# Kernel optimization log

Measured on AMD Instinct MI355X. Metric: run time of the kernel, lower is better.

The kernel has to match this reference:

```python
import jax, jax.numpy as jnp
import numpy as np

B, N, F_IN, F_OUT = 8, 2048, 128, 64
ALPHA = 0.2  # LeakyReLU negative slope
NEG_BIG = -9e15


def setup_inputs() -> dict:
    key = jax.random.key(0)
    k_h, k_adj, k_W, k_a = jax.random.split(key, 4)
    h = jax.random.normal(k_h, (B, N, F_IN), dtype=jnp.float32)
    adj = jax.random.bernoulli(k_adj, 0.1, (N, N)).astype(jnp.float32)
    adj = jnp.maximum(adj, jnp.eye(N, dtype=jnp.float32))
    # xavier_uniform with gain=1.414
    def xavier(k, shape, gain=1.414):
        fan_in, fan_out = shape[0], shape[1]
        bound = gain * np.sqrt(6.0 / (fan_in + fan_out))
        return jax.random.uniform(k, shape, jnp.float32, -bound, bound)
    W = xavier(k_W, (F_IN, F_OUT))
    a = xavier(k_a, (2 * F_OUT, 1))
    return {"h": h, "adj": adj, "W": W, "a": a}


def reference(h, adj, W, a):
    # Wh: [B, N, F_out]
    Wh = jnp.matmul(h, W)
    # a = [a1; a2]; e_ij = leakyrelu(a1.Wh_i + a2.Wh_j) == original concat+matmul
    a1 = a[:F_OUT, 0]
    a2 = a[F_OUT:, 0]
    f = jnp.einsum('bnf,f->bn', Wh, a1)  # [B, N] source term
    g = jnp.einsum('bnf,f->bn', Wh, a2)  # [B, N] target term
    e = jax.nn.leaky_relu(f[:, :, None] + g[:, None, :], negative_slope=ALPHA)  # [B,N,N]
    scores = jnp.where(adj[None, :, :] > 0, e, jnp.float32(NEG_BIG))
    attention = jax.nn.softmax(scores, axis=2)
    # dropout is identity in eval mode (training=False)
    h_prime = jnp.matmul(attention, Wh)  # [B, N, F_out]
    return h_prime
```

## Files before the change

kernel.cpp:

```cpp
#include <hip/hip_runtime.h>
#include <hip/hip_bf16.h>
#include <math.h>

#define B 8
#define N 2048
#define F_IN 128
#define F_OUT 64
#define ALPHA 0.2f

typedef _Float16 half8 __attribute__((ext_vector_type(8)));
typedef float f32x4 __attribute__((ext_vector_type(4)));

__global__ __launch_bounds__(256) void bitmask_kernel(
    const float* __restrict__ adj, unsigned* __restrict__ bits,
    const float* __restrict__ W, const float* __restrict__ a,
    _Float16* __restrict__ Wfrag, float* __restrict__ wa)
{
    const int i = blockIdx.x;
    const int tid = threadIdx.x;
    const int lane = tid & 63;
    const int w = tid >> 6;
    const float* row = adj + (size_t)i * N;
#pragma unroll
    for (int jt = 0; jt < 8; ++jt) {
        float v = row[jt * 256 + tid];
        unsigned long long m = __ballot(v > 0.f);
        if (lane == 0) {
            bits[i * 64 + jt * 8 + w * 2]     = (unsigned)m;
            bits[i * 64 + jt * 8 + w * 2 + 1] = (unsigned)(m >> 32);
        }
    }

    if (blockIdx.x == 0) {
#pragma unroll
        for (int u = 0; u < 32; ++u) {
            int o    = tid * 32 + u;
            int slot = o & 7;
            int ln   = (o >> 3) & 63;
            int fg   = (o >> 9) & 3;
            int ks   = o >> 11;
            int k    = ks * 32 + (ln >> 4) * 8 + slot;
            int f    = fg * 16 + (ln & 15);
            Wfrag[o] = (_Float16)W[k * 64 + f];
        }
        const int k = tid & 127;
        const float* ap = a + (tid >> 7) * 64;
        float s = 0.f;
#pragma unroll
        for (int f = 0; f < 64; ++f) s += W[k * 64 + f] * ap[f];
        wa[(tid >> 7) * 128 + k] = s;
    }
}

__global__ __launch_bounds__(256) void wh_fg_t_kernel(
    const float* __restrict__ h, const _Float16* __restrict__ Wfrag,
    const float* __restrict__ wa, _Float16* __restrict__ Wpack,
    float* __restrict__ fv, float* __restrict__ gv)
{
    const int tid  = threadIdx.x;
    const int w    = tid >> 6;
    const int lane = tid & 63;
    const int mrow = lane & 15;
    const int quad = lane >> 4;

    __shared__ float hs[16 * 132];

    const float4* h4 = (const float4*)(h + (size_t)blockIdx.x * 16 * F_IN);
#pragma unroll
    for (int s = 0; s < 2; ++s) {
        int idx = s * 256 + tid;
        *(float4*)&hs[(idx >> 5) * 132 + (idx & 31) * 4] = h4[idx];
    }

    half8 wF[4];
#pragma unroll
    for (int ks = 0; ks < 4; ++ks)
        wF[ks] = *(const half8*)(Wfrag + (((ks * 4 + w) * 64) + lane) * 8);

    __syncthreads();

    const int jgl = blockIdx.x * 16;
    const int b   = jgl >> 11;
    const int jb  = jgl & (N - 1);
    const float* hrow = &hs[mrow * 132];

    f32x4 acc = {0.f, 0.f, 0.f, 0.f};
#pragma unroll
    for (int ks = 0; ks < 4; ++ks) {
        const float* hp = hrow + ks * 32 + quad * 8;
        float4 x0 = *(const float4*)hp;
        float4 x1 = *(const float4*)(hp + 4);
        half8 aF;
#pragma unroll
        for (int t = 0; t < 4; ++t) {
            aF[t]     = (_Float16)((const float*)&x0)[t];
            aF[4 + t] = (_Float16)((const float*)&x1)[t];
        }
        acc = __builtin_amdgcn_mfma_f32_16x16x32_f16(aF, wF[ks], acc, 0, 0, 0);
    }

    if (w == 0) {
        const float* hp = hrow + quad * 32;
        const float* w1 = wa + quad * 32;
        const float* w2 = wa + 128 + quad * 32;
        float s1 = 0.f, s2 = 0.f;
#pragma unroll
        for (int t = 0; t < 32; ++t) {
            float hv = hp[t];
            s1 += hv * w1[t];
            s2 += hv * w2[t];
        }
        s1 += __shfl_xor(s1, 16, 64); s1 += __shfl_xor(s1, 32, 64);
        s2 += __shfl_xor(s2, 16, 64); s2 += __shfl_xor(s2, 32, 64);
        if (lane < 16) {
            fv[(size_t)b * N + jb + lane] = s1;
            gv[(size_t)b * N + jb + lane] = s2;
        }
    }

    const int m     = jb >> 7;
    const int q     = (jb >> 5) & 3;
    const int jg    = (jb & 31) + quad * 4;
    const int flane = ((jg >> 3) & 3) * 16 + mrow;
    const int slot  = jg & 7;
    _Float16* base = Wpack + ((((size_t)b * 16 + m) * 4 + q) * 4 + w) * 512
                     + (size_t)flane * 8 + slot;
    union { _Float16 hh[4]; ushort4 u; } pk;
#pragma unroll
    for (int reg = 0; reg < 4; ++reg) pk.hh[reg] = (_Float16)acc[reg];
    *(ushort4*)(base) = pk.u;
}

#define MSTR 68
#define RSTR 68

__global__ __launch_bounds__(256) void attn_mfma_kernel(
    const _Float16* __restrict__ Wpack, const float* __restrict__ fv,
    const float* __restrict__ gv, const unsigned* __restrict__ bits,
    float* __restrict__ out)
{
    const int i0 = blockIdx.x * 32;
    const int b  = blockIdx.y;
    const int tid  = threadIdx.x;
    const int lane = tid & 63;
    const int wsl  = tid >> 6;
    const int mrow = lane & 15;
    const int quad = lane >> 4;

    __shared__ __align__(16) float    gs[N];
    __shared__ float    fs[32];
    __shared__ float    ms[32];
    __shared__ __align__(16) unsigned mws[32 * MSTR];
    __shared__ float    redacc[4 * 32 * RSTR];
    __shared__ float    rsp[4 * 32];

    const float4* g4 = (const float4*)(gv + (size_t)b * N);
    ((float4*)gs)[tid]       = g4[tid];
    ((float4*)gs)[tid + 256] = g4[tid + 256];
    if (tid < 32) fs[tid] = fv[(size_t)b * N + i0 + tid];
#pragma unroll
    for (int s = 0; s < 2; ++s) {
        const int idx = tid + s * 256;
        const int i   = idx >> 4;
        const int w4  = (idx & 15) * 4;
        *(uint4*)&mws[i * MSTR + w4] =
            *(const uint4*)&bits[(size_t)(i0 + i) * 64 + w4];
    }
    __syncthreads();

#pragma unroll
    for (int rr = 0; rr < 2; ++rr) {
        const int ii = rr * 16 + (tid >> 4);
        const int jj = tid & 15;
        float gmax = -INFINITY;
#pragma unroll
        for (int t = 0; t < 4; ++t) {
            unsigned mw = mws[ii * MSTR + jj * 4 + t];
            const int jb = jj * 128 + t * 32;
            while (mw) {
                int bit = __builtin_ctz(mw);
                gmax = fmaxf(gmax, gs[jb + bit]);
                mw &= mw - 1;
            }
        }
#pragma unroll
        for (int off = 8; off >= 1; off >>= 1)
            gmax = fmaxf(gmax, __shfl_down(gmax, off, 16));
        if (jj == 0) {
            float m = fs[ii] + gmax;
            ms[ii] = (m > 0.f) ? m : ALPHA * m;
        }
    }
    __syncthreads();

    const float fi0 = fs[mrow],      mi0 = ms[mrow];
    const float fi1 = fs[16 + mrow], mi1 = ms[16 + mrow];
    const _Float16* wpb = Wpack + (size_t)b * 131072;

    f32x4 a00 = {0,0,0,0}, a01 = {0,0,0,0}, a02 = {0,0,0,0}, a03 = {0,0,0,0};
    f32x4 a10 = {0,0,0,0}, a11 = {0,0,0,0}, a12 = {0,0,0,0}, a13 = {0,0,0,0};
    float psum0 = 0.f, psum1 = 0.f;

    for (int mm = 0; mm < 4; ++mm) {
        const int m  = wsl * 4 + mm;
        const uint4 mv0 = *(const uint4*)&mws[mrow * MSTR + m * 4];
        const uint4 mv1 = *(const uint4*)&mws[(16 + mrow) * MSTR + m * 4];
#pragma unroll
        for (int q = 0; q < 4; ++q) {
            const int jb = m * 128 + q * 32 + quad * 8;
            const _Float16* tb = wpb + (size_t)(m * 4 + q) * 2048 + lane * 8;

            half8 b0 = *(const half8*)(tb);
            half8 b1 = *(const half8*)(tb + 512);
            half8 b2 = *(const half8*)(tb + 1024);
            half8 b3 = *(const half8*)(tb + 1536);

            const unsigned w0 = (q == 0) ? mv0.x : (q == 1) ? mv0.y
                               : (q == 2) ? mv0.z : mv0.w;
            const unsigned w1 = (q == 0) ? mv1.x : (q == 1) ? mv1.y
                               : (q == 2) ? mv1.z : mv1.w;
            const unsigned mb0 = (w0 >> (quad * 8)) & 0xFFu;
            const unsigned mb1 = (w1 >> (quad * 8)) & 0xFFu;

            float4 ga = *(const float4*)&gs[jb];
            float4 gb = *(const float4*)&gs[jb + 4];
            half8 aF0, aF1;
#pragma unroll
            for (int t = 0; t < 8; ++t) {
                float g = (t < 4) ? ((const float*)&ga)[t]
                                  : ((const float*)&gb)[t - 4];
                float s0 = fi0 + g; s0 = fmaxf(s0, ALPHA * s0);
                float s1 = fi1 + g; s1 = fmaxf(s1, ALPHA * s1);
                float p0 = ((mb0 >> t) & 1u) ? __expf(s0 - mi0) : 0.f;
                float p1 = ((mb1 >> t) & 1u) ? __expf(s1 - mi1) : 0.f;
                _Float16 h0 = (_Float16)p0, h1 = (_Float16)p1;
                aF0[t] = h0; aF1[t] = h1;
                psum0 += (float)h0; psum1 += (float)h1;
            }

            a00 = __builtin_amdgcn_mfma_f32_16x16x32_f16(aF0, b0, a00, 0, 0, 0);
            a01 = __builtin_amdgcn_mfma_f32_16x16x32_f16(aF0, b1, a01, 0, 0, 0);
            a02 = __builtin_amdgcn_mfma_f32_16x16x32_f16(aF0, b2, a02, 0, 0, 0);
            a03 = __builtin_amdgcn_mfma_f32_16x16x32_f16(aF0, b3, a03, 0, 0, 0);
            a10 = __builtin_amdgcn_mfma_f32_16x16x32_f16(aF1, b0, a10, 0, 0, 0);
            a11 = __builtin_amdgcn_mfma_f32_16x16x32_f16(aF1, b1, a11, 0, 0, 0);
            a12 = __builtin_amdgcn_mfma_f32_16x16x32_f16(aF1, b2, a12, 0, 0, 0);
            a13 = __builtin_amdgcn_mfma_f32_16x16x32_f16(aF1, b3, a13, 0, 0, 0);
        }
    }

    psum0 += __shfl_xor(psum0, 16, 64);
    psum0 += __shfl_xor(psum0, 32, 64);
    psum1 += __shfl_xor(psum1, 16, 64);
    psum1 += __shfl_xor(psum1, 32, 64);
    if (lane < 16) {
        rsp[wsl * 32 + lane]      = psum0;
        rsp[wsl * 32 + 16 + lane] = psum1;
    }

#pragma unroll
    for (int reg = 0; reg < 4; ++reg) {
        const int r0 = quad * 4 + reg;
        float* d0 = &redacc[(wsl * 32 + r0) * RSTR];
        d0[mrow]      = a00[reg];
        d0[16 + mrow] = a01[reg];
        d0[32 + mrow] = a02[reg];
        d0[48 + mrow] = a03[reg];
        float* d1 = &redacc[(wsl * 32 + 16 + r0) * RSTR];
        d1[mrow]      = a10[reg];
        d1[16 + mrow] = a11[reg];
        d1[32 + mrow] = a12[reg];
        d1[48 + mrow] = a13[reg];
    }
    __syncthreads();

    const int col  = tid & 63;
    const int rgrp = tid >> 6;
#pragma unroll
    for (int rr = 0; rr < 8; ++rr) {
        const int row = rgrp * 8 + rr;
        float sum = redacc[(row) * RSTR + col]
                  + redacc[(32 + row) * RSTR + col]
                  + redacc[(64 + row) * RSTR + col]
                  + redacc[(96 + row) * RSTR + col];
        float den = rsp[row] + rsp[32 + row] + rsp[64 + row] + rsp[96 + row];
        out[((size_t)b * N + i0 + row) * F_OUT + col] = sum / den;
    }
}

extern "C" void kernel_launch(void* const* d_in, const int* in_sizes, int n_in,
                              void* d_out, int out_size, void* d_ws, size_t ws_size,
                              hipStream_t stream) {
    const float* h   = (const float*)d_in[0];
    const float* adj = (const float*)d_in[1];
    const float* W   = (const float*)d_in[2];
    const float* a   = (const float*)d_in[3];
    float* out = (float*)d_out;

    char* ws = (char*)d_ws;
    _Float16* Wpack = (_Float16*)ws;
    float* fv = (float*)(ws + (size_t)B * F_OUT * N * 2);
    float* gv = fv + (size_t)B * N;
    unsigned* bits = (unsigned*)(gv + (size_t)B * N);
    _Float16* Wfrag = (_Float16*)((char*)bits + (size_t)N * 64 * 4);
    float* wa = (float*)(Wfrag + 8192);

    bitmask_kernel<<<dim3(N), 256, 0, stream>>>(adj, bits, W, a, Wfrag, wa);
    wh_fg_t_kernel<<<dim3(B * N / 16), 256, 0, stream>>>(h, Wfrag, wa, Wpack, fv, gv);
    attn_mfma_kernel<<<dim3(N / 32, B), 256, 0, stream>>>(Wpack, fv, gv, bits, out);
}
```

Baseline: 102.1 us.

## Fuse bitmask and Wh kernels, use exp2 with prescaled logits, MFMA row sums

Merges the adjacency-bitmask kernel and the Wh/f/g projection kernel into one launch. Blocks are split by blockIdx, and each projection block recomputes W·a and its W fragments directly from W, so the serial dependency on block 0 disappears. In the attention kernel, f and g are prescaled by log2(e) so the exponent can use the native exp2. The per-lane softmax denominator sums and their shuffles are replaced by two extra MFMAs against a ones vector. The cost is redundant W reads and W·a dot products in every projection block, plus two more MFMAs per inner step.

```diff
diff --git a/kernel.cpp b/kernel.cpp
--- a/kernel.cpp
+++ b/kernel.cpp
@@ -7,79 +7,78 @@
 #define F_IN 128
 #define F_OUT 64
 #define ALPHA 0.2f
+#define LOG2E 1.4426950408889634f
+
+#if __has_builtin(__builtin_amdgcn_exp2f)
+#define EXP2F(x) __builtin_amdgcn_exp2f(x)
+#else
+#define EXP2F(x) exp2f(x)
+#endif
 
 typedef _Float16 half8 __attribute__((ext_vector_type(8)));
 typedef float f32x4 __attribute__((ext_vector_type(4)));
 
-__global__ __launch_bounds__(256) void bitmask_kernel(
+__global__ __launch_bounds__(256) void fused_pre_kernel(
     const float* __restrict__ adj, unsigned* __restrict__ bits,
-    const float* __restrict__ W, const float* __restrict__ a,
-    _Float16* __restrict__ Wfrag, float* __restrict__ wa)
-{
-    const int i = blockIdx.x;
-    const int tid = threadIdx.x;
-    const int lane = tid & 63;
-    const int w = tid >> 6;
-    const float* row = adj + (size_t)i * N;
-#pragma unroll
-    for (int jt = 0; jt < 8; ++jt) {
-        float v = row[jt * 256 + tid];
-        unsigned long long m = __ballot(v > 0.f);
-        if (lane == 0) {
-            bits[i * 64 + jt * 8 + w * 2]     = (unsigned)m;
-            bits[i * 64 + jt * 8 + w * 2 + 1] = (unsigned)(m >> 32);
-        }
-    }
-
-    if (blockIdx.x == 0) {
-#pragma unroll
-        for (int u = 0; u < 32; ++u) {
-            int o    = tid * 32 + u;
-            int slot = o & 7;
-            int ln   = (o >> 3) & 63;
-            int fg   = (o >> 9) & 3;
-            int ks   = o >> 11;
-            int k    = ks * 32 + (ln >> 4) * 8 + slot;
-            int f    = fg * 16 + (ln & 15);
-            Wfrag[o] = (_Float16)W[k * 64 + f];
-        }
-        const int k = tid & 127;
-        const float* ap = a + (tid >> 7) * 64;
-        float s = 0.f;
-#pragma unroll
-        for (int f = 0; f < 64; ++f) s += W[k * 64 + f] * ap[f];
-        wa[(tid >> 7) * 128 + k] = s;
-    }
-}
-
-__global__ __launch_bounds__(256) void wh_fg_t_kernel(
-    const float* __restrict__ h, const _Float16* __restrict__ Wfrag,
-    const float* __restrict__ wa, _Float16* __restrict__ Wpack,
+    const float* __restrict__ h, const float* __restrict__ W,
+    const float* __restrict__ a, _Float16* __restrict__ Wpack,
     float* __restrict__ fv, float* __restrict__ gv)
 {
-    const int tid  = threadIdx.x;
+    const int tid = threadIdx.x;
+
+    __shared__ float hs[16 * 132];
+    __shared__ float was[256];
+
+    if (blockIdx.x < N) {
+        const int i = blockIdx.x;
+        const int lane = tid & 63;
+        const int w = tid >> 6;
+        const float* row = adj + (size_t)i * N;
+#pragma unroll
+        for (int jt = 0; jt < 8; ++jt) {
+            float v = row[jt * 256 + tid];
+            unsigned long long m = __ballot(v > 0.f);
+            if (lane == 0) {
+                bits[i * 64 + jt * 8 + w * 2]     = (unsigned)m;
+                bits[i * 64 + jt * 8 + w * 2 + 1] = (unsigned)(m >> 32);
+            }
+        }
+        return;
+    }
+
+    const int blk  = blockIdx.x - N;
     const int w    = tid >> 6;
     const int lane = tid & 63;
     const int mrow = lane & 15;
     const int quad = lane >> 4;
 
-    __shared__ float hs[16 * 132];
-
-    const float4* h4 = (const float4*)(h + (size_t)blockIdx.x * 16 * F_IN);
+    const float4* h4 = (const float4*)(h + (size_t)blk * 16 * F_IN);
 #pragma unroll
     for (int s = 0; s < 2; ++s) {
         int idx = s * 256 + tid;
         *(float4*)&hs[(idx >> 5) * 132 + (idx & 31) * 4] = h4[idx];
     }
 
+    {
+        const int k = tid & 127;
+        const float* ap = a + (tid >> 7) * 64;
+        const float* wr = W + k * 64;
+        float s = 0.f;
+#pragma unroll
+        for (int f = 0; f < 64; ++f) s += wr[f] * ap[f];
+        was[(tid >> 7) * 128 + k] = s;
+    }
+
     half8 wF[4];
 #pragma unroll
     for (int ks = 0; ks < 4; ++ks)
-        wF[ks] = *(const half8*)(Wfrag + (((ks * 4 + w) * 64) + lane) * 8);
+#pragma unroll
+        for (int slot = 0; slot < 8; ++slot)
+            wF[ks][slot] = (_Float16)W[(ks * 32 + quad * 8 + slot) * 64 + w * 16 + mrow];
 
     __syncthreads();
 
-    const int jgl = blockIdx.x * 16;
+    const int jgl = blk * 16;
     const int b   = jgl >> 11;
     const int jb  = jgl & (N - 1);
     const float* hrow = &hs[mrow * 132];
@@ -101,8 +100,8 @@
 
     if (w == 0) {
         const float* hp = hrow + quad * 32;
-        const float* w1 = wa + quad * 32;
-        const float* w2 = wa + 128 + quad * 32;
+        const float* w1 = &was[quad * 32];
+        const float* w2 = &was[128 + quad * 32];
         float s1 = 0.f, s2 = 0.f;
 #pragma unroll
         for (int t = 0; t < 32; ++t) {
@@ -155,9 +154,13 @@
     __shared__ float    rsp[4 * 32];
 
     const float4* g4 = (const float4*)(gv + (size_t)b * N);
-    ((float4*)gs)[tid]       = g4[tid];
-    ((float4*)gs)[tid + 256] = g4[tid + 256];
-    if (tid < 32) fs[tid] = fv[(size_t)b * N + i0 + tid];
+#pragma unroll
+    for (int s = 0; s < 2; ++s) {
+        float4 gvv = g4[tid + s * 256];
+        gvv.x *= LOG2E; gvv.y *= LOG2E; gvv.z *= LOG2E; gvv.w *= LOG2E;
+        ((float4*)gs)[tid + s * 256] = gvv;
+    }
+    if (tid < 32) fs[tid] = fv[(size_t)b * N + i0 + tid] * LOG2E;
 #pragma unroll
     for (int s = 0; s < 2; ++s) {
         const int idx = tid + s * 256;
@@ -197,9 +200,13 @@
     const float fi1 = fs[16 + mrow], mi1 = ms[16 + mrow];
     const _Float16* wpb = Wpack + (size_t)b * 131072;
 
+    half8 ones;
+#pragma unroll
+    for (int t = 0; t < 8; ++t) ones[t] = (_Float16)1.0f;
+
     f32x4 a00 = {0,0,0,0}, a01 = {0,0,0,0}, a02 = {0,0,0,0}, a03 = {0,0,0,0};
     f32x4 a10 = {0,0,0,0}, a11 = {0,0,0,0}, a12 = {0,0,0,0}, a13 = {0,0,0,0};
-    float psum0 = 0.f, psum1 = 0.f;
+    f32x4 s0acc = {0,0,0,0}, s1acc = {0,0,0,0};
 
     for (int mm = 0; mm < 4; ++mm) {
         const int m  = wsl * 4 + mm;
@@ -231,11 +238,10 @@
                                   : ((const float*)&gb)[t - 4];
                 float s0 = fi0 + g; s0 = fmaxf(s0, ALPHA * s0);
                 float s1 = fi1 + g; s1 = fmaxf(s1, ALPHA * s1);
-                float p0 = ((mb0 >> t) & 1u) ? __expf(s0 - mi0) : 0.f;
-                float p1 = ((mb1 >> t) & 1u) ? __expf(s1 - mi1) : 0.f;
-                _Float16 h0 = (_Float16)p0, h1 = (_Float16)p1;
-                aF0[t] = h0; aF1[t] = h1;
-                psum0 += (float)h0; psum1 += (float)h1;
+                float p0 = ((mb0 >> t) & 1u) ? EXP2F(s0 - mi0) : 0.f;
+                float p1 = ((mb1 >> t) & 1u) ? EXP2F(s1 - mi1) : 0.f;
+                aF0[t] = (_Float16)p0;
+                aF1[t] = (_Float16)p1;
             }
 
             a00 = __builtin_amdgcn_mfma_f32_16x16x32_f16(aF0, b0, a00, 0, 0, 0);
@@ -246,16 +252,17 @@
             a11 = __builtin_amdgcn_mfma_f32_16x16x32_f16(aF1, b1, a11, 0, 0, 0);
             a12 = __builtin_amdgcn_mfma_f32_16x16x32_f16(aF1, b2, a12, 0, 0, 0);
             a13 = __builtin_amdgcn_mfma_f32_16x16x32_f16(aF1, b3, a13, 0, 0, 0);
-        }
-    }
-
-    psum0 += __shfl_xor(psum0, 16, 64);
-    psum0 += __shfl_xor(psum0, 32, 64);
-    psum1 += __shfl_xor(psum1, 16, 64);
-    psum1 += __shfl_xor(psum1, 32, 64);
-    if (lane < 16) {
-        rsp[wsl * 32 + lane]      = psum0;
-        rsp[wsl * 32 + 16 + lane] = psum1;
+            s0acc = __builtin_amdgcn_mfma_f32_16x16x32_f16(aF0, ones, s0acc, 0, 0, 0);
+            s1acc = __builtin_amdgcn_mfma_f32_16x16x32_f16(aF1, ones, s1acc, 0, 0, 0);
+        }
+    }
+
+    if (mrow == 0) {
+#pragma unroll
+        for (int reg = 0; reg < 4; ++reg) {
+            rsp[wsl * 32 + quad * 4 + reg]      = s0acc[reg];
+            rsp[wsl * 32 + 16 + quad * 4 + reg] = s1acc[reg];
+        }
     }
 
 #pragma unroll
@@ -302,10 +309,8 @@
     float* fv = (float*)(ws + (size_t)B * F_OUT * N * 2);
     float* gv = fv + (size_t)B * N;
     unsigned* bits = (unsigned*)(gv + (size_t)B * N);
-    _Float16* Wfrag = (_Float16*)((char*)bits + (size_t)N * 64 * 4);
-    float* wa = (float*)(Wfrag + 8192);
-
-    bitmask_kernel<<<dim3(N), 256, 0, stream>>>(adj, bits, W, a, Wfrag, wa);
-    wh_fg_t_kernel<<<dim3(B * N / 16), 256, 0, stream>>>(h, Wfrag, wa, Wpack, fv, gv);
+
+    fused_pre_kernel<<<dim3(N + B * N / 16), 256, 0, stream>>>(
+        adj, bits, h, W, a, Wpack, fv, gv);
     attn_mfma_kernel<<<dim3(N / 32, B), 256, 0, stream>>>(Wpack, fv, gv, bits, out);
 }
```

Result: slower. 113.0 us (+10.7%).
